# Performance work log

Hardware: AMD Instinct MI355X
Metric: run time of the kernel (lower is better)

The kernel has to match this reference:

```python
import jax, jax.numpy as jnp
import numpy as np

H = 128          # hidden_size
GX = GY = 512    # grid_size
SW = 2           # spatial_width
NX = GX + 3 * SW # memory extent x (as in SpatialExternalMemory ctor)
NY = GY + 3 * SW
B = 512          # batch (num trajectories)
T = 64           # seq len (recurrent steps)


def setup_inputs() -> dict:
    key = jax.random.key(0)
    ks = jax.random.split(key, 9)
    stdv = 1.0 / np.sqrt(H)
    feat = jax.random.normal(ks[0], (B, T, 2), jnp.float32)
    # integer grid coords stored as floats in cols 2:4 (cast to long in forward)
    coords = jax.random.randint(ks[1], (B, T, 2), 0, GX).astype(jnp.float32)
    feature_tensor = jnp.concatenate([feat, coords], axis=-1)  # [B, T, 4]
    seq_lengths = jax.random.randint(ks[2], (B,), 1, T + 1)
    uni = lambda k, shp: jax.random.uniform(k, shp, jnp.float32, -stdv, stdv)
    return {
        "feature_tensor": feature_tensor,
        "W_ih": uni(ks[3], (4 * H, 2)),
        "b_ih": uni(ks[4], (4 * H,)),
        "W_hh": uni(ks[5], (4 * H, H)),
        "b_hh": uni(ks[6], (4 * H,)),
        "W_out": uni(ks[7], (H, 2 * H)),   # Attention.linear_out: [H, 2H]
        "b_out": uni(ks[8], (H,)),
        "seq_lengths": seq_lengths,
    }


def reference(feature_tensor, W_ih, b_ih, W_hh, b_hh, W_out, b_out, seq_lengths):
    step_idx = jnp.maximum(seq_lengths.astype(jnp.int32), 1) - 1  # [B]
    offsets = jnp.arange(-SW, SW + 1)                              # [K], K=2*SW+1
    K = 2 * SW + 1
    memory0 = jnp.zeros((NX, NY, H), jnp.float32)
    hidden0 = jnp.zeros((B, H), jnp.float32)
    last0 = jnp.zeros((B, H), jnp.float32)

    def step(carry, inp):
        hidden, memory, last = carry
        xt, t = inp                                 # xt: [B,4]
        feat = xt[:, :2]
        grid = xt[:, 2:4].astype(jnp.int32) + SW    # [B,2]
        gi = feat @ W_ih.T + b_ih                   # [B,4H]
        gh = hidden @ W_hh.T + b_hh                 # [B,4H]
        i_r, i_i, i_n, i_s = jnp.split(gi, 4, axis=1)
        h_r, h_i, h_n, h_s = jnp.split(gh, 4, axis=1)
        resetgate = jax.nn.sigmoid(i_r + h_r)
        updategate = jax.nn.sigmoid(i_i + h_i)
        spatialgate = jax.nn.sigmoid(i_s + h_s)
        newgate = jnp.tanh(i_n + resetgate * h_n)
        # --- find_nearby_grids: 5x5 neighborhood gather ---
        gx = jnp.clip(grid[:, 0], 0, NX - 1)
        gy = jnp.clip(grid[:, 1], 0, NY - 1)
        xi = jnp.clip(gx[:, None] + offsets[None, :], 0, NX - 1)   # [B,K]
        yi = jnp.clip(gy[:, None] + offsets[None, :], 0, NY - 1)   # [B,K]
        xg = jnp.broadcast_to(xi[:, :, None], (B, K, K)).reshape(B, K * K)
        yg = jnp.broadcast_to(yi[:, None, :], (B, K, K)).reshape(B, K * K)
        context = memory[xg, yg]                    # [B, K*K, H]
        # --- Attention(newgate.detach(), context) ---
        q = jax.lax.stop_gradient(newgate)
        scores = jnp.einsum('bh,bkh->bk', q, context)
        scores = jnp.where(scores == 0.0, -jnp.inf, scores)
        attn = jax.nn.softmax(scores, axis=1)
        attn = jnp.where(jnp.isnan(attn), 0.0, attn)
        mix = jnp.einsum('bk,bkh->bh', attn, context)
        atten_cs = jnp.tanh(jnp.concatenate([mix, q], axis=-1) @ W_out.T + b_out)
        curr = newgate + spatialgate * atten_cs
        out = curr + updategate * (hidden - curr)
        # --- in-cell memory write (detached, training-mode path) ---
        sd = jax.lax.stop_gradient(spatialgate)
        od = jax.lax.stop_gradient(out)
        upd = sd * memory[gx, gy] + (1.0 - sd) * od
        memory = memory.at[gx, gy].set(upd)
        last = jnp.where((step_idx == t)[:, None], out, last)
        return (out, memory, last), None

    xs = (jnp.swapaxes(feature_tensor, 0, 1), jnp.arange(T))
    (_, _, last), _ = jax.lax.scan(step, (hidden0, memory0, last0), xs)
    return last
```

## Files before the change

kernel.cpp:

```cpp
#include <hip/hip_runtime.h>
#include <hip/hip_fp16.h>
#include <math.h>

#define Hc   128
#define Bc   512
#define Tc   64
#define NXc  518
#define NCELL (518*518)
#define NEV  (Bc*Tc)
#define SWc  2


__global__ void k_build(const float* __restrict__ feat, int* __restrict__ head,
                        int* __restrict__ nxt, int* __restrict__ cellxy) {
    int gid = blockIdx.x * 256 + threadIdx.x;
    if (gid >= NEV) return;
    int b = gid >> 6, t = gid & 63;
    int base = (b * Tc + t) * 4;
    int gx = (int)feat[base + 2] + SWc;
    int gy = (int)feat[base + 3] + SWc;
    gx = min(max(gx, 0), NXc - 1);
    gy = min(max(gy, 0), NXc - 1);
    int cell = gx * NXc + gy;
    int e = t * Bc + b;
    cellxy[e] = (gx << 16) | gy;
    int old = atomicExch(&head[cell], e);
    nxt[e] = old;
}

__global__ void k_resolve(const int* __restrict__ head, const int* __restrict__ nxt,
                          const int* __restrict__ cellxy, int* __restrict__ dep) {
    int gid = blockIdx.x * 256 + threadIdx.x;
    if (gid >= NEV * 25) return;
    int r = gid / 25, k = gid - r * 25;
    int t = r & 63, b = r >> 6;
    int e0 = t * Bc + b;
    int xy = cellxy[e0];
    int gx = xy >> 16, gy = xy & 0xffff;
    int cx = gx + (k / 5) - SWc, cy = gy + (k % 5) - SWc;
    cx = min(max(cx, 0), NXc - 1);
    cy = min(max(cy, 0), NXc - 1);
    int cell = cx * NXc + cy;
    int best = -1;
    for (int e = head[cell]; e >= 0; e = nxt[e])
        if ((e >> 9) < t && e > best) best = e;
    dep[r * 25 + k] = best;
}


#define LOG2E 1.4426950408889634f
__device__ __forceinline__ float fexp(float x)  { return __builtin_amdgcn_exp2f(x * LOG2E); }
__device__ __forceinline__ float fsig(float x)  { return __builtin_amdgcn_rcpf(1.f + fexp(-x)); }
__device__ __forceinline__ float ftanh(float x) { return 1.f - 2.f * __builtin_amdgcn_rcpf(1.f + fexp(2.f * x)); }

template <int CTRL>
__device__ __forceinline__ float dppadd(float x) {
    int t = __builtin_amdgcn_update_dpp(0, __float_as_int(x), CTRL, 0xF, 0xF, true);
    return x + __int_as_float(t);
}
template <int CTRL>
__device__ __forceinline__ float dppmax(float x) {
    int t = __builtin_amdgcn_update_dpp(0, __float_as_int(x), CTRL, 0xF, 0xF, true);
    return fmaxf(x, __int_as_float(t));
}
__device__ __forceinline__ float swz16(float x) {
    return __int_as_float(__builtin_amdgcn_ds_swizzle(__float_as_int(x), 0x401F));
}
__device__ __forceinline__ float redsum64(float d) {
    d = dppadd<0xB1>(d); d = dppadd<0x4E>(d);
    d = dppadd<0x141>(d); d = dppadd<0x140>(d);
    d += swz16(d);
    d += __shfl_xor(d, 32, 64);
    return d;
}

__device__ __forceinline__ void barlds() {
    asm volatile("" ::: "memory");
    __builtin_amdgcn_s_waitcnt(0xC07F);
    __builtin_amdgcn_s_barrier();
    asm volatile("" ::: "memory");
}


constexpr int LDS_FLOATS = 16512 + 256 + 1024 + 256 + 256 + 64 + 512 + 16 + 128 + 256 + 128;
constexpr int LDS_BYTES  = LDS_FLOATS * 4;

__global__ void
__attribute__((amdgpu_flat_work_group_size(1024, 1024)))
__attribute__((amdgpu_waves_per_eu(4, 4)))
step_main(const float* __restrict__ feat, const float* __restrict__ Wih,
          const float* __restrict__ bih,  const float* __restrict__ Whh,
          const float* __restrict__ bhh,  const float* __restrict__ Wout,
          const float* __restrict__ bout, const int*   __restrict__ seq,
          const int*   __restrict__ dep,  float* __restrict__ vbuf,
          unsigned*    __restrict__ flags, float* __restrict__ dout) {
    extern __shared__ float lds[];
    __half2* WoutH = (__half2*)lds;
    float* hid   = lds + 16512;
    float* g     = hid   + 256;
    float* gin   = g     + 1024;
    float* ctr   = gin   + 256;
    float* scor  = ctr   + 256;
    float* catL  = scor  + 64;
    float* fxy   = catL  + 512;
    float* boutL = fxy   + 16;
    float* updL  = boutL + 128;
    int*   depv  = (int*)(updL + 256);

    const int tid  = threadIdx.x;
    const int blk  = blockIdx.x;
    const int lane = tid & 63;
    const int w    = tid >> 6;
    const int wj   = w >> 3;
    const int ww   = w & 7;

    const int rp = tid >> 2;
    const int q  = tid & 3;
    const int r0 = 2 * rp, r1 = 2 * rp + 1;
    float4 wr0[8], wr1[8];
    {
        const float4* w0 = (const float4*)(Whh + (size_t)r0 * Hc);
        const float4* w1 = (const float4*)(Whh + (size_t)r1 * Hc);
        #pragma unroll
        for (int i = 0; i < 8; ++i) { wr0[i] = w0[q + 4 * i]; wr1[i] = w1[q + 4 * i]; }
    }
    #pragma unroll
    for (int i = 0; i < 8; ++i) {
        asm volatile("" : "+v"(wr0[i].x), "+v"(wr0[i].y), "+v"(wr0[i].z), "+v"(wr0[i].w));
        asm volatile("" : "+v"(wr1[i].x), "+v"(wr1[i].y), "+v"(wr1[i].z), "+v"(wr1[i].w));
    }
    const int jw = q & 1;
    const int rw = r0 + (q >> 1);
    const float bihr = bih[rw], bhhr = bhh[rw];
    const float wihA = Wih[rw * 2 + 0], wihB = Wih[rw * 2 + 1];
    const int chunk = rw >> 7;

    for (int i = tid; i < 128 * 128; i += 1024) {
        int r = i >> 7, c2 = i & 127;
        WoutH[r * 129 + c2] = __floats2half2_rn(Wout[r * 256 + 2 * c2],
                                                Wout[r * 256 + 2 * c2 + 1]);
    }
    if (tid < 128) boutL[tid] = bout[tid];
    if (tid < 256) hid[tid] = 0.f;
    if (tid < 8) { int j = tid >> 2, c = tid & 3;
                   fxy[tid] = feat[((size_t)(blk * 2 + j) * Tc + 0) * 4 + c]; }
    if (tid < 50) {
        int j = (tid >= 25), k = tid - j * 25;
        depv[tid] = dep[(((size_t)(blk * 2 + j)) * Tc + 0) * 25 + k];
    }
    const int s0 = max(seq[blk * 2 + 0], 1) - 1;
    const int s1 = max(seq[blk * 2 + 1], 1) - 1;
    __syncthreads();

    const float NEG_INF = -__builtin_inff();

    for (int t = 0; t < Tc; ++t) {
        const float* fx = fxy + (t & 1) * 8;
        int* depvCur = depv + (t & 1) * 64;
        int* depvNxt = depv + ((t + 1) & 1) * 64;

        if (t > 0 && (w == 0 || w == 2)) {
            int j = w >> 1;
            float2 u = *(const float2*)&updL[j * 128 + 2 * lane];
            unsigned long long raw; __builtin_memcpy(&raw, &u, 8);
            __hip_atomic_store((unsigned long long*)(vbuf +
                ((size_t)((t - 1) * Bc + blk * 2 + j)) * Hc + 2 * lane),
                raw, __ATOMIC_RELAXED, __HIP_MEMORY_SCOPE_AGENT);
        }
        const int mye = (lane < 25) ? depvCur[wj * 25 + lane] : -1;
        unsigned fpre = 1u;
        if (mye >= 0)
            fpre = __hip_atomic_load(&flags[mye], __ATOMIC_RELAXED,
                                     __HIP_MEMORY_SCOPE_AGENT);

        float a00 = 0.f, a01 = 0.f, a10 = 0.f, a11 = 0.f;
        {
            const float4* h0 = (const float4*)hid;
            const float4* h1 = (const float4*)(hid + 128);
            #pragma unroll
            for (int i = 0; i < 8; ++i) {
                float4 hv0 = h0[q + 4 * i], hv1 = h1[q + 4 * i];
                float4 w0 = wr0[i], w1 = wr1[i];
                a00 = fmaf(w0.x, hv0.x, fmaf(w0.y, hv0.y, fmaf(w0.z, hv0.z, fmaf(w0.w, hv0.w, a00))));
                a01 = fmaf(w1.x, hv0.x, fmaf(w1.y, hv0.y, fmaf(w1.z, hv0.z, fmaf(w1.w, hv0.w, a01))));
                a10 = fmaf(w0.x, hv1.x, fmaf(w0.y, hv1.y, fmaf(w0.z, hv1.z, fmaf(w0.w, hv1.w, a10))));
                a11 = fmaf(w1.x, hv1.x, fmaf(w1.y, hv1.y, fmaf(w1.z, hv1.z, fmaf(w1.w, hv1.w, a11))));
            }
        }
        a00 = dppadd<0x4E>(dppadd<0xB1>(a00));
        a01 = dppadd<0x4E>(dppadd<0xB1>(a01));
        a10 = dppadd<0x4E>(dppadd<0xB1>(a10));
        a11 = dppadd<0x4E>(dppadd<0xB1>(a11));
        {
            float mine = (q & 1) ? ((q >> 1) ? a11 : a10) : ((q >> 1) ? a01 : a00);
            float gi  = fmaf(wihA, fx[jw * 4 + 0], wihB * fx[jw * 4 + 1]);
            g[jw * 512 + rw] = mine + bhhr + ((chunk == 2) ? 0.f : (gi + bihr));
            if (chunk == 2) gin[jw * 128 + (rw & 127)] = gi + bihr;
        }
        if (tid >= 512 && tid < 562 && t + 1 < Tc) {
            int idx = tid - 512;
            int j = (idx >= 25), k = idx - j * 25;
            depvNxt[idx] = dep[(((size_t)(blk * 2 + j)) * Tc + (t + 1)) * 25 + k];
        }
        if (tid >= 960 && tid < 968 && t + 1 < Tc) {
            int idx = tid - 960, j = idx >> 2, c = idx & 3;
            fxy[((t + 1) & 1) * 8 + idx] =
                feat[((size_t)(blk * 2 + j) * Tc + (t + 1)) * 4 + c];
        }
        if (t > 0 && (w == 0 || w == 2)) {
            asm volatile("s_waitcnt vmcnt(0)" ::: "memory");
            if (lane == 0)
                __hip_atomic_store(&flags[(t - 1) * Bc + blk * 2 + (w >> 1)], 1u,
                                   __ATOMIC_RELAXED, __HIP_MEMORY_SCOPE_AGENT);
        }
        {
            bool pend = (mye >= 0) && (fpre == 0u);
            while (__any(pend)) {
                if (pend && __hip_atomic_load(&flags[mye], __ATOMIC_RELAXED,
                                              __HIP_MEMORY_SCOPE_AGENT) != 0u)
                    pend = false;
                if (__any(pend)) __builtin_amdgcn_s_sleep(1);
            }
        }
        asm volatile("" ::: "memory");
        float2 valk[4];
        int    evk[4];
        #pragma unroll
        for (int kk = 0; kk < 4; ++kk) {
            int k = ww + 8 * kk;
            evk[kk] = (k < 25) ? depvCur[wj * 25 + k] : -1;
            valk[kk] = make_float2(0.f, 0.f);
            if (evk[kk] >= 0)
                valk[kk] = *(const float2*)(vbuf + (size_t)evk[kk] * Hc + 2 * lane);
        }
        barlds();

        float q0, q1;
        {
            float2 gr2 = *(const float2*)&g[wj * 512 + 2 * lane];
            float2 gn2 = *(const float2*)&g[wj * 512 + 256 + 2 * lane];
            float2 gi2 = *(const float2*)&gin[wj * 128 + 2 * lane];
            q0 = ftanh(gi2.x + fsig(gr2.x) * gn2.x);
            q1 = ftanh(gi2.y + fsig(gr2.y) * gn2.y);
        }
        if (ww == 0) *(float2*)&catL[wj * 256 + 128 + 2 * lane] = make_float2(q0, q1);
        if (ww == 1) *(float2*)&catL[wj * 256 + 2 * lane] = make_float2(0.f, 0.f);
        if (ww == 4)
            *(float2*)&ctr[wj * 128 + 2 * lane] =
                (evk[1] >= 0) ? valk[1] : make_float2(0.f, 0.f);
        #pragma unroll
        for (int kk = 0; kk < 4; ++kk) {
            int k = ww + 8 * kk;
            if (k < 25) {
                float sc;
                if (evk[kk] >= 0) {
                    float d = fmaf(valk[kk].x, q0, valk[kk].y * q1);
                    d = redsum64(d);
                    sc = (d == 0.f) ? NEG_INF : d;
                } else sc = NEG_INF;
                if (lane == 0) scor[wj * 32 + k] = sc;
            }
        }
        barlds();

        {
            int k2 = lane & 31;
            float v = (k2 < 25) ? scor[wj * 32 + k2] : NEG_INF;
            float m = v;
            m = dppmax<0xB1>(m); m = dppmax<0x4E>(m);
            m = dppmax<0x141>(m); m = dppmax<0x140>(m);
            m = fmaxf(m, swz16(m));
            float a = 0.f;
            if (m != NEG_INF) {
                float p = (v == NEG_INF) ? 0.f : fexp(v - m);
                float s = p;
                s = dppadd<0xB1>(s); s = dppadd<0x4E>(s);
                s = dppadd<0x141>(s); s = dppadd<0x140>(s);
                s += swz16(s);
                a = p / s;
            }
            if ((evk[0] >= 0) | (evk[1] >= 0) | (evk[2] >= 0) | (evk[3] >= 0)) {
                float pm0 = 0.f, pm1 = 0.f;
                #pragma unroll
                for (int kk = 0; kk < 4; ++kk) {
                    int k = ww + 8 * kk;
                    if (k < 25 && evk[kk] >= 0) {
                        float ak = __int_as_float(
                            __builtin_amdgcn_readlane(__float_as_int(a), k));
                        pm0 = fmaf(ak, valk[kk].x, pm0);
                        pm1 = fmaf(ak, valk[kk].y, pm1);
                    }
                }
                atomicAdd(&catL[wj * 256 + 2 * lane],     pm0);
                atomicAdd(&catL[wj * 256 + 2 * lane + 1], pm1);
            }
        }
        barlds();

        {
            const int oi = lane & 7, p = lane >> 3;
            const int oo = 8 * w + oi;
            const __half2* wrow = WoutH + oo * 129 + p * 16;
            const float4* cat4 = (const float4*)catL;
            float acc0 = 0.f, acc1 = 0.f;
            #pragma unroll
            for (int c = 0; c < 8; ++c) {
                int cc = (c + p) & 7;
                __half2 wa = wrow[2 * cc], wb = wrow[2 * cc + 1];
                float wx = __low2float(wa), wy = __high2float(wa);
                float wz = __low2float(wb), wv = __high2float(wb);
                float4 v0 = cat4[p * 8 + cc];
                float4 v1 = cat4[64 + p * 8 + cc];
                acc0 = fmaf(wx, v0.x, fmaf(wy, v0.y, fmaf(wz, v0.z, fmaf(wv, v0.w, acc0))));
                acc1 = fmaf(wx, v1.x, fmaf(wy, v1.y, fmaf(wz, v1.z, fmaf(wv, v1.w, acc1))));
            }
            acc0 = dppadd<0x128>(acc0); acc0 += swz16(acc0); acc0 += __shfl_xor(acc0, 32, 64);
            acc1 = dppadd<0x128>(acc1); acc1 += swz16(acc1); acc1 += __shfl_xor(acc1, 32, 64);
            if (lane < 8) {
                #pragma unroll
                for (int j = 0; j < 2; ++j) {
                    float tot = ((j == 0) ? acc0 : acc1) + boutL[oo];
                    float at = ftanh(tot);
                    float gr = g[j * 512 + oo],       gu = g[j * 512 + 128 + oo];
                    float gn = g[j * 512 + 256 + oo], gs = g[j * 512 + 384 + oo];
                    float rr = fsig(gr), uu = fsig(gu), ss = fsig(gs);
                    float nn = ftanh(gin[j * 128 + oo] + rr * gn);
                    float hv = hid[j * 128 + oo];
                    float curr = fmaf(ss, at, nn);
                    float outv = curr + uu * (hv - curr);
                    hid[j * 128 + oo] = outv;
                    if (t < Tc - 1)
                        updL[j * 128 + oo] = fmaf(ss, ctr[j * 128 + oo], (1.f - ss) * outv);
                    int sj = (j == 0) ? s0 : s1;
                    if (sj == t) dout[(size_t)(blk * 2 + j) * Hc + oo] = outv;
                }
            }
        }
        barlds();
    }
}


extern "C" void kernel_launch(void* const* d_in, const int* in_sizes, int n_in,
                              void* d_out, int out_size, void* d_ws, size_t ws_size,
                              hipStream_t stream) {
    const float* feat = (const float*)d_in[0];
    const float* Wih  = (const float*)d_in[1];
    const float* bih  = (const float*)d_in[2];
    const float* Whh  = (const float*)d_in[3];
    const float* bhh  = (const float*)d_in[4];
    const float* Wout = (const float*)d_in[5];
    const float* bout = (const float*)d_in[6];
    const int*   seq  = (const int*)d_in[7];

    char* ws = (char*)d_ws;
    size_t off = 0;
    auto carve = [&](size_t bytes) { char* p = ws + off; off += (bytes + 511) & ~(size_t)511; return p; };
    float*    vbuf   = (float*)   carve((size_t)NEV * Hc * 4);
    int*      head   = (int*)     carve((size_t)NCELL * 4);
    int*      nxt    = (int*)     carve((size_t)NEV * 4);
    int*      cellxy = (int*)     carve((size_t)NEV * 4);
    int*      dep    = (int*)     carve((size_t)NEV * 25 * 4);
    unsigned* flags  = (unsigned*)carve((size_t)NEV * 4);

    hipMemsetAsync(head, 0xFF, (size_t)NCELL * 4, stream);
    hipMemsetAsync(flags, 0, (size_t)NEV * 4, stream);

    k_build<<<(NEV + 255) / 256, 256, 0, stream>>>(feat, head, nxt, cellxy);
    k_resolve<<<(NEV * 25 + 255) / 256, 256, 0, stream>>>(head, nxt, cellxy, dep);

    hipFuncSetAttribute((const void*)step_main,
                        hipFuncAttributeMaxDynamicSharedMemorySize, LDS_BYTES);
    step_main<<<256, 1024, LDS_BYTES, stream>>>(feat, Wih, bih, Whh, bhh, Wout, bout,
                                                seq, dep, vbuf, flags, (float*)d_out);
}
```

Baseline: 504.1 us.

## Prefetch dependency flags for next step, per-k wait, and replace LDS atomics with reduction

Each wave now reads the readiness flags of the next step's dependency events early and keeps them in a register. When a dependency was already ready it issues the vbuf loads before the recurrent matvec instead of after the spin-wait. The spin-wait now polls per neighbour slot and reloads only the values that were not ready. The attention-mix accumulation no longer uses LDS float atomicAdd. Each wave writes partial sums to a new LDS buffer, and an extra barrier and pass over 256 threads reduce them. This costs about 8KB more LDS and one more barrier per step.

```diff
diff --git a/kernel.cpp b/kernel.cpp
--- a/kernel.cpp
+++ b/kernel.cpp
@@ -81,8 +81,12 @@
     asm volatile("" ::: "memory");
 }
 
-
-constexpr int LDS_FLOATS = 16512 + 256 + 1024 + 256 + 256 + 64 + 512 + 16 + 128 + 256 + 128;
+__device__ __forceinline__ unsigned flagload(const unsigned* p) {
+    return __hip_atomic_load(p, __ATOMIC_RELAXED, __HIP_MEMORY_SCOPE_AGENT);
+}
+
+
+constexpr int LDS_FLOATS = 16512 + 256 + 1024 + 256 + 256 + 64 + 2048 + 512 + 16 + 128 + 256 + 128;
 constexpr int LDS_BYTES  = LDS_FLOATS * 4;
 
 __global__ void
@@ -101,7 +105,8 @@
     float* gin   = g     + 1024;
     float* ctr   = gin   + 256;
     float* scor  = ctr   + 256;
-    float* catL  = scor  + 64;
+    float* pmix  = scor  + 64;
+    float* catL  = pmix  + 2048;
     float* fxy   = catL  + 512;
     float* boutL = fxy   + 16;
     float* updL  = boutL + 128;
@@ -154,6 +159,8 @@
 
     const float NEG_INF = -__builtin_inff();
 
+    unsigned fnextv = 0u;
+
     for (int t = 0; t < Tc; ++t) {
         const float* fx = fxy + (t & 1) * 8;
         int* depvCur = depv + (t & 1) * 64;
@@ -167,11 +174,16 @@
                 ((size_t)((t - 1) * Bc + blk * 2 + j)) * Hc + 2 * lane),
                 raw, __ATOMIC_RELAXED, __HIP_MEMORY_SCOPE_AGENT);
         }
-        const int mye = (lane < 25) ? depvCur[wj * 25 + lane] : -1;
-        unsigned fpre = 1u;
-        if (mye >= 0)
-            fpre = __hip_atomic_load(&flags[mye], __ATOMIC_RELAXED,
-                                     __HIP_MEMORY_SCOPE_AGENT);
+        int evk[4]; bool rdy[4]; float2 valk[4];
+        #pragma unroll
+        for (int kk = 0; kk < 4; ++kk) {
+            int k = ww + 8 * kk;
+            evk[kk] = (k < 25) ? depvCur[wj * 25 + k] : -1;
+            rdy[kk] = (__builtin_amdgcn_readlane(fnextv, kk) != 0) && (evk[kk] >= 0);
+            valk[kk] = make_float2(0.f, 0.f);
+            if (rdy[kk])
+                valk[kk] = *(const float2*)(vbuf + (size_t)evk[kk] * Hc + 2 * lane);
+        }
 
         float a00 = 0.f, a01 = 0.f, a10 = 0.f, a11 = 0.f;
         {
@@ -214,24 +226,23 @@
                                    __ATOMIC_RELAXED, __HIP_MEMORY_SCOPE_AGENT);
         }
         {
-            bool pend = (mye >= 0) && (fpre == 0u);
-            while (__any(pend)) {
-                if (pend && __hip_atomic_load(&flags[mye], __ATOMIC_RELAXED,
-                                              __HIP_MEMORY_SCOPE_AGENT) != 0u)
-                    pend = false;
-                if (__any(pend)) __builtin_amdgcn_s_sleep(1);
-            }
-        }
-        asm volatile("" ::: "memory");
-        float2 valk[4];
-        int    evk[4];
-        #pragma unroll
-        for (int kk = 0; kk < 4; ++kk) {
-            int k = ww + 8 * kk;
-            evk[kk] = (k < 25) ? depvCur[wj * 25 + k] : -1;
-            valk[kk] = make_float2(0.f, 0.f);
-            if (evk[kk] >= 0)
-                valk[kk] = *(const float2*)(vbuf + (size_t)evk[kk] * Hc + 2 * lane);
+            bool p0 = (evk[0] >= 0) && !rdy[0];
+            bool p1 = (evk[1] >= 0) && !rdy[1];
+            bool p2 = (evk[2] >= 0) && !rdy[2];
+            bool p3 = (evk[3] >= 0) && !rdy[3];
+            bool n0 = p0, n1 = p1, n2 = p2, n3 = p3;
+            while (p0 | p1 | p2 | p3) {
+                if (p0 && flagload(&flags[evk[0]]) != 0u) p0 = false;
+                if (p1 && flagload(&flags[evk[1]]) != 0u) p1 = false;
+                if (p2 && flagload(&flags[evk[2]]) != 0u) p2 = false;
+                if (p3 && flagload(&flags[evk[3]]) != 0u) p3 = false;
+                if (p0 | p1 | p2 | p3) __builtin_amdgcn_s_sleep(1);
+            }
+            asm volatile("" ::: "memory");
+            if (n0) valk[0] = *(const float2*)(vbuf + (size_t)evk[0] * Hc + 2 * lane);
+            if (n1) valk[1] = *(const float2*)(vbuf + (size_t)evk[1] * Hc + 2 * lane);
+            if (n2) valk[2] = *(const float2*)(vbuf + (size_t)evk[2] * Hc + 2 * lane);
+            if (n3) valk[3] = *(const float2*)(vbuf + (size_t)evk[3] * Hc + 2 * lane);
         }
         barlds();
 
@@ -244,7 +255,6 @@
             q1 = ftanh(gi2.y + fsig(gr2.y) * gn2.y);
         }
         if (ww == 0) *(float2*)&catL[wj * 256 + 128 + 2 * lane] = make_float2(q0, q1);
-        if (ww == 1) *(float2*)&catL[wj * 256 + 2 * lane] = make_float2(0.f, 0.f);
         if (ww == 4)
             *(float2*)&ctr[wj * 128 + 2 * lane] =
                 (evk[1] >= 0) ? valk[1] : make_float2(0.f, 0.f);
@@ -264,6 +274,14 @@
         barlds();
 
         {
+            if (t + 1 < Tc && lane < 4) {
+                int k = ww + 8 * lane;
+                int e = (k < 25) ? depvNxt[wj * 25 + k] : -1;
+                fnextv = (e >= 0) ? flagload(&flags[e]) : 0u;
+            } else if (lane < 4) {
+                fnextv = 0u;
+            }
+
             int k2 = lane & 31;
             float v = (k2 < 25) ? scor[wj * 32 + k2] : NEG_INF;
             float m = v;
@@ -279,21 +297,27 @@
                 s += swz16(s);
                 a = p / s;
             }
-            if ((evk[0] >= 0) | (evk[1] >= 0) | (evk[2] >= 0) | (evk[3] >= 0)) {
-                float pm0 = 0.f, pm1 = 0.f;
-                #pragma unroll
-                for (int kk = 0; kk < 4; ++kk) {
-                    int k = ww + 8 * kk;
-                    if (k < 25 && evk[kk] >= 0) {
-                        float ak = __int_as_float(
-                            __builtin_amdgcn_readlane(__float_as_int(a), k));
-                        pm0 = fmaf(ak, valk[kk].x, pm0);
-                        pm1 = fmaf(ak, valk[kk].y, pm1);
-                    }
+            float pm0 = 0.f, pm1 = 0.f;
+            #pragma unroll
+            for (int kk = 0; kk < 4; ++kk) {
+                int k = ww + 8 * kk;
+                if (k < 25 && evk[kk] >= 0) {
+                    float ak = __int_as_float(
+                        __builtin_amdgcn_readlane(__float_as_int(a), k));
+                    pm0 = fmaf(ak, valk[kk].x, pm0);
+                    pm1 = fmaf(ak, valk[kk].y, pm1);
                 }
-                atomicAdd(&catL[wj * 256 + 2 * lane],     pm0);
-                atomicAdd(&catL[wj * 256 + 2 * lane + 1], pm1);
-            }
+            }
+            *(float2*)&pmix[(wj * 8 + ww) * 128 + 2 * lane] = make_float2(pm0, pm1);
+        }
+        barlds();
+
+        if (tid < 256) {
+            int j = tid >> 7, h = tid & 127;
+            float mix = 0.f;
+            #pragma unroll
+            for (int p = 0; p < 8; ++p) mix += pmix[(j * 8 + p) * 128 + h];
+            catL[j * 256 + h] = mix;
         }
         barlds();
 
```

Result: slower. 630.4 us (+25.0%).

## Keep Wout fp16 weights in registers and replace LDS atomics with partial-mix reduction

Applied to the files above, without the earlier changes.

Each thread now holds its slice of the fp16-packed W_out in 16 registers, and bout in one, instead of staging the whole matrix in LDS. This frees about 66KB of shared memory and removes LDS reads in the output projection. The attention mix accumulation no longer uses LDS atomicAdd into catL: each wave writes its partial sums to a pmix buffer, and a separate pass reduces them and copies the query vector into catL. This removes atomic contention but adds one more barrier per step and raises register pressure under a fixed waves-per-EU setting.

```diff
diff --git a/kernel.cpp b/kernel.cpp
--- a/kernel.cpp
+++ b/kernel.cpp
@@ -81,8 +81,12 @@
     asm volatile("" ::: "memory");
 }
 
-
-constexpr int LDS_FLOATS = 16512 + 256 + 1024 + 256 + 256 + 64 + 512 + 16 + 128 + 256 + 128;
+__device__ __forceinline__ unsigned flagload(const unsigned* p) {
+    return __hip_atomic_load(p, __ATOMIC_RELAXED, __HIP_MEMORY_SCOPE_AGENT);
+}
+
+
+constexpr int LDS_FLOATS = 256 + 1024 + 256 + 256 + 256 + 64 + 2048 + 512 + 16 + 256 + 128;
 constexpr int LDS_BYTES  = LDS_FLOATS * 4;
 
 __global__ void
@@ -95,16 +99,16 @@
           const int*   __restrict__ dep,  float* __restrict__ vbuf,
           unsigned*    __restrict__ flags, float* __restrict__ dout) {
     extern __shared__ float lds[];
-    __half2* WoutH = (__half2*)lds;
-    float* hid   = lds + 16512;
+    float* hid   = lds;
     float* g     = hid   + 256;
     float* gin   = g     + 1024;
     float* ctr   = gin   + 256;
-    float* scor  = ctr   + 256;
-    float* catL  = scor  + 64;
+    float* qvL   = ctr   + 256;
+    float* scor  = qvL   + 256;
+    float* pmix  = scor  + 64;
+    float* catL  = pmix  + 2048;
     float* fxy   = catL  + 512;
-    float* boutL = fxy   + 16;
-    float* updL  = boutL + 128;
+    float* updL  = fxy   + 16;
     int*   depv  = (int*)(updL + 256);
 
     const int tid  = threadIdx.x;
@@ -135,12 +139,21 @@
     const float wihA = Wih[rw * 2 + 0], wihB = Wih[rw * 2 + 1];
     const int chunk = rw >> 7;
 
-    for (int i = tid; i < 128 * 128; i += 1024) {
-        int r = i >> 7, c2 = i & 127;
-        WoutH[r * 129 + c2] = __floats2half2_rn(Wout[r * 256 + 2 * c2],
-                                                Wout[r * 256 + 2 * c2 + 1]);
-    }
-    if (tid < 128) boutL[tid] = bout[tid];
+    const int oi = lane & 7, p = lane >> 3;
+    const int oo = 8 * w + oi;
+    unsigned wo[16];
+    {
+        const float* wrow = Wout + (size_t)oo * 256 + p * 32;
+        #pragma unroll
+        for (int m = 0; m < 16; ++m) {
+            __half2 hh = __floats2half2_rn(wrow[2 * m], wrow[2 * m + 1]);
+            unsigned u; __builtin_memcpy(&u, &hh, 4);
+            wo[m] = u;
+            asm volatile("" : "+v"(wo[m]));
+        }
+    }
+    const float boutr = bout[oo];
+
     if (tid < 256) hid[tid] = 0.f;
     if (tid < 8) { int j = tid >> 2, c = tid & 3;
                    fxy[tid] = feat[((size_t)(blk * 2 + j) * Tc + 0) * 4 + c]; }
@@ -170,8 +183,7 @@
         const int mye = (lane < 25) ? depvCur[wj * 25 + lane] : -1;
         unsigned fpre = 1u;
         if (mye >= 0)
-            fpre = __hip_atomic_load(&flags[mye], __ATOMIC_RELAXED,
-                                     __HIP_MEMORY_SCOPE_AGENT);
+            fpre = flagload(&flags[mye]);
 
         float a00 = 0.f, a01 = 0.f, a10 = 0.f, a11 = 0.f;
         {
@@ -216,8 +228,7 @@
         {
             bool pend = (mye >= 0) && (fpre == 0u);
             while (__any(pend)) {
-                if (pend && __hip_atomic_load(&flags[mye], __ATOMIC_RELAXED,
-                                              __HIP_MEMORY_SCOPE_AGENT) != 0u)
+                if (pend && flagload(&flags[mye]) != 0u)
                     pend = false;
                 if (__any(pend)) __builtin_amdgcn_s_sleep(1);
             }
@@ -243,8 +254,7 @@
             q0 = ftanh(gi2.x + fsig(gr2.x) * gn2.x);
             q1 = ftanh(gi2.y + fsig(gr2.y) * gn2.y);
         }
-        if (ww == 0) *(float2*)&catL[wj * 256 + 128 + 2 * lane] = make_float2(q0, q1);
-        if (ww == 1) *(float2*)&catL[wj * 256 + 2 * lane] = make_float2(0.f, 0.f);
+        if (ww == 0) *(float2*)&qvL[wj * 128 + 2 * lane] = make_float2(q0, q1);
         if (ww == 4)
             *(float2*)&ctr[wj * 128 + 2 * lane] =
                 (evk[1] >= 0) ? valk[1] : make_float2(0.f, 0.f);
@@ -272,43 +282,49 @@
             m = fmaxf(m, swz16(m));
             float a = 0.f;
             if (m != NEG_INF) {
-                float p = (v == NEG_INF) ? 0.f : fexp(v - m);
-                float s = p;
+                float pr = (v == NEG_INF) ? 0.f : fexp(v - m);
+                float s = pr;
                 s = dppadd<0xB1>(s); s = dppadd<0x4E>(s);
                 s = dppadd<0x141>(s); s = dppadd<0x140>(s);
                 s += swz16(s);
-                a = p / s;
-            }
-            if ((evk[0] >= 0) | (evk[1] >= 0) | (evk[2] >= 0) | (evk[3] >= 0)) {
-                float pm0 = 0.f, pm1 = 0.f;
-                #pragma unroll
-                for (int kk = 0; kk < 4; ++kk) {
-                    int k = ww + 8 * kk;
-                    if (k < 25 && evk[kk] >= 0) {
-                        float ak = __int_as_float(
-                            __builtin_amdgcn_readlane(__float_as_int(a), k));
-                        pm0 = fmaf(ak, valk[kk].x, pm0);
-                        pm1 = fmaf(ak, valk[kk].y, pm1);
-                    }
+                a = pr / s;
+            }
+            float pm0 = 0.f, pm1 = 0.f;
+            #pragma unroll
+            for (int kk = 0; kk < 4; ++kk) {
+                int k = ww + 8 * kk;
+                if (k < 25 && evk[kk] >= 0) {
+                    float ak = __int_as_float(
+                        __builtin_amdgcn_readlane(__float_as_int(a), k));
+                    pm0 = fmaf(ak, valk[kk].x, pm0);
+                    pm1 = fmaf(ak, valk[kk].y, pm1);
                 }
-                atomicAdd(&catL[wj * 256 + 2 * lane],     pm0);
-                atomicAdd(&catL[wj * 256 + 2 * lane + 1], pm1);
-            }
-        }
-        barlds();
-
-        {
-            const int oi = lane & 7, p = lane >> 3;
-            const int oo = 8 * w + oi;
-            const __half2* wrow = WoutH + oo * 129 + p * 16;
+            }
+            *(float2*)&pmix[(wj * 8 + ww) * 128 + 2 * lane] = make_float2(pm0, pm1);
+        }
+        barlds();
+
+        if (tid < 256) {
+            int j = tid >> 7, h = tid & 127;
+            float mix = 0.f;
+            #pragma unroll
+            for (int pp = 0; pp < 8; ++pp) mix += pmix[(j * 8 + pp) * 128 + h];
+            catL[j * 256 + h] = mix;
+            catL[j * 256 + 128 + h] = qvL[j * 128 + h];
+        }
+        barlds();
+
+        {
             const float4* cat4 = (const float4*)catL;
             float acc0 = 0.f, acc1 = 0.f;
             #pragma unroll
             for (int c = 0; c < 8; ++c) {
                 int cc = (c + p) & 7;
-                __half2 wa = wrow[2 * cc], wb = wrow[2 * cc + 1];
+                unsigned ua = wo[2 * cc], ub = wo[2 * cc + 1];
+                __half2 wa, wb2;
+                __builtin_memcpy(&wa, &ua, 4); __builtin_memcpy(&wb2, &ub, 4);
                 float wx = __low2float(wa), wy = __high2float(wa);
-                float wz = __low2float(wb), wv = __high2float(wb);
+                float wz = __low2float(wb2), wv = __high2float(wb2);
                 float4 v0 = cat4[p * 8 + cc];
                 float4 v1 = cat4[64 + p * 8 + cc];
                 acc0 = fmaf(wx, v0.x, fmaf(wy, v0.y, fmaf(wz, v0.z, fmaf(wv, v0.w, acc0))));
@@ -319,7 +335,7 @@
             if (lane < 8) {
                 #pragma unroll
                 for (int j = 0; j < 2; ++j) {
-                    float tot = ((j == 0) ? acc0 : acc1) + boutL[oo];
+                    float tot = ((j == 0) ? acc0 : acc1) + boutr;
                     float at = ftanh(tot);
                     float gr = g[j * 512 + oo],       gu = g[j * 512 + 128 + oo];
                     float gn = g[j * 512 + 256 + oo], gs = g[j * 512 + 384 + oo];
```

New measurement: 429.6 us, median of 2. 14.8% less time.
